# Optimization experiments

Measured on AMD Instinct MI355X. Metric: run time of the kernel, lower is better.

Reference implementation:

```python
import jax, jax.numpy as jnp
import numpy as np

B, N, C, H = 2, 2048, 1024, 16
D = C // H  # head_dim = 64


def setup_inputs() -> dict:
    key = jax.random.key(0)
    ks = jax.random.split(key, 5)
    s = 1.0 / np.sqrt(C)
    return {
        "q": jax.random.normal(ks[0], (B, N, C), dtype=jnp.float32),
        "W_qkv": jax.random.normal(ks[1], (C, 3 * C), dtype=jnp.float32) * s,
        "b_qkv": jnp.zeros((3 * C,), dtype=jnp.float32),
        "W_proj": jax.random.normal(ks[2], (C, C), dtype=jnp.float32) * s,
        "b_proj": jnp.zeros((C,), dtype=jnp.float32),
    }


def reference(q, W_qkv, b_qkv, W_proj, b_proj):
    # Self-attention: k = v = q. Full 3C projection (as in the torch code).
    qkv = q @ W_qkv + b_qkv  # [B, N, 3C]
    qh = qkv[:, :, :C].reshape(B, N, H, D)
    kh = qkv[:, :, C:2 * C].reshape(B, N, H, D)
    vh = qkv[:, :, 2 * C:].reshape(B, N, H, D)
    scale = D ** -0.5
    # [B, H, N, N] attention logits
    attn = jnp.einsum("bnhd,bmhd->bhnm", qh, kh) * scale
    attn = jax.nn.softmax(attn, axis=-1)
    out = jnp.einsum("bhnm,bmhd->bnhd", attn, vh).reshape(B, N, C)
    return out @ W_proj + b_proj
```

## Files before the change

### kernel.cpp

```cpp
#include <hip/hip_runtime.h>
#include <stdint.h>

typedef __bf16 bf16_t;
typedef __bf16 bf16x8 __attribute__((ext_vector_type(8)));
typedef __bf16 bf16x4 __attribute__((ext_vector_type(4)));
typedef float f32x4 __attribute__((ext_vector_type(4)));

#define L2E 1.44269504088896340736f
#define QSCALE (0.125f * L2E)

__device__ __forceinline__ void gload16(const bf16_t* g, bf16_t* l) {
  __builtin_amdgcn_global_load_lds(
      (const __attribute__((address_space(1))) void*)g,
      (__attribute__((address_space(3))) void*)l, 16, 0, 0);
}

__global__ __launch_bounds__(256) void cast_q_kernel(const float* __restrict__ in,
                                                     bf16_t* __restrict__ out) {
  int i = blockIdx.x * 256 + threadIdx.x;
  float4 v = reinterpret_cast<const float4*>(in)[i];
  bf16x4 o;
  o[0] = (bf16_t)v.x; o[1] = (bf16_t)v.y; o[2] = (bf16_t)v.z; o[3] = (bf16_t)v.w;
  reinterpret_cast<bf16x4*>(out)[i] = o;
}

__global__ __launch_bounds__(256) void transpose_cast_kernel(const float* __restrict__ in,
                                                             bf16_t* __restrict__ out,
                                                             int K, int N) {
  __shared__ float tile[64][65];
  int k0 = blockIdx.y * 64, n0 = blockIdx.x * 64;
  int t = threadIdx.x;
  int r = t >> 4, c4 = (t & 15) * 4;
#pragma unroll
  for (int rr = 0; rr < 4; rr++) {
    int row = r + rr * 16;
    float4 v = *reinterpret_cast<const float4*>(&in[(size_t)(k0 + row) * N + n0 + c4]);
    tile[row][c4 + 0] = v.x; tile[row][c4 + 1] = v.y;
    tile[row][c4 + 2] = v.z; tile[row][c4 + 3] = v.w;
  }
  __syncthreads();
#pragma unroll
  for (int rr = 0; rr < 4; rr++) {
    int nr = r + rr * 16;
    bf16x4 o;
#pragma unroll
    for (int i = 0; i < 4; i++) o[i] = (bf16_t)tile[c4 + i][nr];
    *reinterpret_cast<bf16x4*>(&out[(size_t)(n0 + nr) * K + k0 + c4]) = o;
  }
}

template <int MODE>
__global__ __launch_bounds__(256) void gemm_kernel(const bf16_t* __restrict__ A,
                                                   const bf16_t* __restrict__ Bt,
                                                   const float* __restrict__ bias,
                                                   void* __restrict__ out,
                                                   bf16_t* __restrict__ vT,
                                                   int K, int gm, int gn, int ldo) {
  __shared__ __align__(16) bf16_t smem[17408];
  bf16_t* At = smem;
  bf16_t* Bts = smem + 8192;
  const int t = threadIdx.x, lane = t & 63, w = t >> 6;
  const int g = lane >> 4, q = lane & 15;
  const int bid = blockIdx.x, x = bid & 7, r = bid >> 3;
  const int qm = gm >> 2, qn = gn >> 1;
  const int lm = r % qm, ln = r / qm;
  const int m0 = ((x & 3) * qm + lm) * 128, n0 = ((x >> 2) * qn + ln) * 128;
  const int wm = (w >> 1) * 64, wn = (w & 1) * 64;

  const bf16_t* srcA[4]; const bf16_t* srcB[4]; int dsto[4];
#pragma unroll
  for (int i = 0; i < 4; i++) {
    int gI = i * 256 + t;
    int row = gI >> 3, p = (gI & 7) ^ (row & 7);
    srcA[i] = A + (size_t)(m0 + row) * K + p * 8;
    srcB[i] = Bt + (size_t)(n0 + row) * K + p * 8;
    dsto[i] = (i * 256 + w * 64) * 8;
  }

  f32x4 acc[4][4];
#pragma unroll
  for (int i = 0; i < 4; i++)
#pragma unroll
    for (int j = 0; j < 4; j++) acc[i][j] = (f32x4){0.f, 0.f, 0.f, 0.f};

  for (int k0 = 0; k0 < K; k0 += 64) {
    __syncthreads();
#pragma unroll
    for (int i = 0; i < 4; i++) {
      gload16(srcA[i] + k0, &At[dsto[i]]);
      gload16(srcB[i] + k0, &Bts[dsto[i]]);
    }
    __syncthreads();
#pragma unroll
    for (int dc = 0; dc < 2; dc++) {
      bf16x8 am[4], bn[4];
#pragma unroll
      for (int i = 0; i < 4; i++) {
        int ra = wm + 16 * i + q;
        am[i] = *reinterpret_cast<const bf16x8*>(&At[ra * 64 + ((dc * 32 + g * 8) ^ ((ra & 7) * 8))]);
        int rb = wn + 16 * i + q;
        bn[i] = *reinterpret_cast<const bf16x8*>(&Bts[rb * 64 + ((dc * 32 + g * 8) ^ ((rb & 7) * 8))]);
      }
      __builtin_amdgcn_s_setprio(1);
#pragma unroll
      for (int i = 0; i < 4; i++)
#pragma unroll
        for (int j = 0; j < 4; j++)
          acc[i][j] = __builtin_amdgcn_mfma_f32_16x16x32_bf16(am[i], bn[j], acc[i][j], 0, 0, 0);
      __builtin_amdgcn_s_setprio(0);
    }
  }

  if (MODE == 0 && n0 >= 2048) {
    __syncthreads();
    bf16_t* TT = smem;
#pragma unroll
    for (int i = 0; i < 4; i++)
#pragma unroll
      for (int j = 0; j < 4; j++)
#pragma unroll
        for (int rr = 0; rr < 4; rr++) {
          int ch = wn + 16 * j + q;
          int tok = wm + 16 * i + 4 * g + rr;
          float v = acc[i][j][rr] + bias[n0 + ch];
          TT[ch * 136 + (((tok >> 3) ^ (ch & 7)) * 8) + (tok & 7)] = (bf16_t)v;
        }
    __syncthreads();
    const int bb = m0 >> 11;
    const int t0 = m0 & 2047;
#pragma unroll
    for (int it = 0; it < 8; it++) {
      int ch = it * 16 + w * 4 + (lane >> 4);
      int ck = lane & 15;
      uint4 val = *reinterpret_cast<const uint4*>(&TT[ch * 136 + ((ck ^ (ch & 7)) * 8)]);
      int vch = (n0 - 2048) + ch;
      bf16_t* dst = vT + ((size_t)(bb * 16 + (vch >> 6)) * 64 + (vch & 63)) * 2048 + t0 + ck * 8;
      *reinterpret_cast<uint4*>(dst) = val;
    }
  } else {
#pragma unroll
    for (int i = 0; i < 4; i++)
#pragma unroll
      for (int j = 0; j < 4; j++)
#pragma unroll
        for (int rr = 0; rr < 4; rr++) {
          int row = m0 + wm + 16 * i + 4 * g + rr;
          int col = n0 + wn + 16 * j + q;
          float v = acc[i][j][rr] + bias[col];
          if (MODE == 0) {
            if (col < 1024) v *= QSCALE;
            ((bf16_t*)out)[(size_t)row * ldo + col] = (bf16_t)v;
          } else {
            ((float*)out)[(size_t)row * ldo + col] = v;
          }
        }
  }
}

__global__ __launch_bounds__(256) void attn_kernel(const bf16_t* __restrict__ qk,
                                                   const bf16_t* __restrict__ vT,
                                                   bf16_t* __restrict__ aout) {
  __shared__ __align__(16) bf16_t sK[2][4096];
  __shared__ __align__(16) bf16_t sV[2][4096];
  __shared__ __align__(16) bf16_t sP[4][1024];

  const int t = threadIdx.x, lane = t & 63, w = t >> 6;
  const int g = lane >> 4, q = lane & 15;
  const int bid = blockIdx.x, xr = bid >> 3;
  const int bh = (bid & 7) * 4 + (xr >> 5);
  const int b = bh >> 4, h = bh & 15;
  const int q0 = (xr & 31) * 64 + w * 16;
  const bf16_t* qk_b = qk + (size_t)b * 2048 * 2048;
  const bf16_t* vT_h = vT + (size_t)bh * 64 * 2048;
  bf16_t* Pw = sP[w];

  const bf16_t* srcK[2]; const bf16_t* srcV[2]; int dsto[2];
#pragma unroll
  for (int i = 0; i < 2; i++) {
    int gI = (w * 2 + i) * 64 + lane;
    int row = gI >> 3, p = (gI & 7) ^ (row & 7);
    srcK[i] = qk_b + (size_t)row * 2048 + 1024 + h * 64 + p * 8;
    srcV[i] = vT_h + (size_t)row * 2048 + p * 8;
    dsto[i] = (w * 2 + i) * 512;
  }

  bf16x8 bq[2];
  {
    const bf16_t* qr = qk_b + (size_t)(q0 + q) * 2048 + h * 64;
    bq[0] = *reinterpret_cast<const bf16x8*>(qr + g * 8);
    bq[1] = *reinterpret_cast<const bf16x8*>(qr + 32 + g * 8);
  }

  bf16x8 ones;
#pragma unroll
  for (int i = 0; i < 8; i++) ones[i] = (bf16_t)1.0f;

  f32x4 oacc[4];
#pragma unroll
  for (int c = 0; c < 4; c++) oacc[c] = (f32x4){0.f, 0.f, 0.f, 0.f};
  f32x4 lacc = (f32x4){0.f, 0.f, 0.f, 0.f};

#pragma unroll
  for (int i = 0; i < 2; i++) {
    gload16(srcK[i], &sK[0][dsto[i]]);
    gload16(srcV[i], &sV[0][dsto[i]]);
  }
  __syncthreads();

  for (int tt = 0; tt < 32; tt++) {
    const int cur = tt & 1;
    if (tt + 1 < 32) {
      size_t koffK = (size_t)(tt + 1) * 64 * 2048;
      size_t koffV = (size_t)(tt + 1) * 64;
#pragma unroll
      for (int i = 0; i < 2; i++) {
        gload16(srcK[i] + koffK, &sK[cur ^ 1][dsto[i]]);
        gload16(srcV[i] + koffV, &sV[cur ^ 1][dsto[i]]);
      }
    }

    const bf16_t* Kc = sK[cur];
    f32x4 s[4];
    __builtin_amdgcn_s_setprio(1);
#pragma unroll
    for (int c = 0; c < 4; c++) {
      int row = 16 * c + q, sw = (q & 7) * 8;
      bf16x8 ka0 = *reinterpret_cast<const bf16x8*>(&Kc[row * 64 + ((g * 8) ^ sw)]);
      bf16x8 ka1 = *reinterpret_cast<const bf16x8*>(&Kc[row * 64 + ((32 + g * 8) ^ sw)]);
      f32x4 z = (f32x4){0.f, 0.f, 0.f, 0.f};
      z = __builtin_amdgcn_mfma_f32_16x16x32_bf16(ka0, bq[0], z, 0, 0, 0);
      z = __builtin_amdgcn_mfma_f32_16x16x32_bf16(ka1, bq[1], z, 0, 0, 0);
      s[c] = z;
    }
    __builtin_amdgcn_s_setprio(0);

#pragma unroll
    for (int c = 0; c < 4; c++) {
      bf16x4 pk;
#pragma unroll
      for (int rr = 0; rr < 4; rr++) pk[rr] = (bf16_t)exp2f(s[c][rr]);
      *reinterpret_cast<bf16x4*>(
          &Pw[q * 64 + (((2 * c + (g >> 1)) ^ (q & 7)) * 8) + (g & 1) * 4]) = pk;
    }

    const bf16_t* Vc = sV[cur];
    __builtin_amdgcn_s_setprio(1);
#pragma unroll
    for (int kc = 0; kc < 2; kc++) {
      bf16x8 pb = *reinterpret_cast<const bf16x8*>(
          &Pw[q * 64 + (((kc * 4 + g) ^ (q & 7)) * 8)]);
      lacc = __builtin_amdgcn_mfma_f32_16x16x32_bf16(ones, pb, lacc, 0, 0, 0);
#pragma unroll
      for (int c = 0; c < 4; c++) {
        int row = 16 * c + q;
        bf16x8 va = *reinterpret_cast<const bf16x8*>(
            &Vc[row * 64 + (((kc * 4 + g) ^ (q & 7)) * 8)]);
        oacc[c] = __builtin_amdgcn_mfma_f32_16x16x32_bf16(va, pb, oacc[c], 0, 0, 0);
      }
    }
    __builtin_amdgcn_s_setprio(0);

    __syncthreads();
  }

  float inv = 1.0f / lacc[0];
  bf16_t* orow = aout + (size_t)(b * 2048 + q0 + q) * 1024 + h * 64;
#pragma unroll
  for (int c = 0; c < 4; c++) {
    bf16x4 ov;
#pragma unroll
    for (int rr = 0; rr < 4; rr++) ov[rr] = (bf16_t)(oacc[c][rr] * inv);
    *reinterpret_cast<bf16x4*>(orow + c * 16 + g * 4) = ov;
  }
}

extern "C" void kernel_launch(void* const* d_in, const int* in_sizes, int n_in,
                              void* d_out, int out_size, void* d_ws, size_t ws_size,
                              hipStream_t stream) {
  const float* q     = (const float*)d_in[0];
  const float* Wqkv  = (const float*)d_in[1];
  const float* bqkv  = (const float*)d_in[2];
  const float* Wproj = (const float*)d_in[3];
  const float* bproj = (const float*)d_in[4];
  float* out = (float*)d_out;

  char* ws = (char*)d_ws;
  bf16_t* q_bf    = (bf16_t*)(ws);
  bf16_t* wqkv_t  = (bf16_t*)(ws + 8388608);
  bf16_t* wproj_t = (bf16_t*)(ws + 14680064);
  bf16_t* qk      = (bf16_t*)(ws + 16777216);
  bf16_t* vT      = (bf16_t*)(ws + 33554432);
  bf16_t* aout    = q_bf;

  cast_q_kernel<<<4096, 256, 0, stream>>>(q, q_bf);
  transpose_cast_kernel<<<dim3(48, 16), 256, 0, stream>>>(Wqkv, wqkv_t, 1024, 3072);
  transpose_cast_kernel<<<dim3(16, 16), 256, 0, stream>>>(Wproj, wproj_t, 1024, 1024);
  gemm_kernel<0><<<768, 256, 0, stream>>>(q_bf, wqkv_t, bqkv, qk, vT, 1024, 32, 24, 2048);
  attn_kernel<<<1024, 256, 0, stream>>>(qk, vT, aout);
  gemm_kernel<1><<<256, 256, 0, stream>>>(aout, wproj_t, bproj, out, nullptr, 1024, 32, 8, 1024);
}
```

Before: 149.4 us.

## Process two query sub-tiles per attention wave and use smaller projection GEMM tiles

Measured after the change: 145.6 us. -2.6%, faster.

```diff
diff --git a/kernel.cpp b/kernel.cpp
--- a/kernel.cpp
+++ b/kernel.cpp
@@ -49,61 +49,68 @@
   }
 }
 
-template <int MODE>
+template <int MODE, int BM>
 __global__ __launch_bounds__(256) void gemm_kernel(const bf16_t* __restrict__ A,
                                                    const bf16_t* __restrict__ Bt,
                                                    const float* __restrict__ bias,
                                                    void* __restrict__ out,
                                                    bf16_t* __restrict__ vT,
                                                    int K, int gm, int gn, int ldo) {
-  __shared__ __align__(16) bf16_t smem[17408];
+  constexpr int ACH = BM / 8;
+  constexpr int NCH = ACH + 16;
+  constexpr int CPW = NCH / 4;
+  constexpr int IR = BM / 32;
+  constexpr int SMEM = (MODE == 0) ? 17408 : (BM * 64 + 8192);
+  __shared__ __align__(16) bf16_t smem[SMEM];
   bf16_t* At = smem;
-  bf16_t* Bts = smem + 8192;
+  bf16_t* Bts = smem + BM * 64;
   const int t = threadIdx.x, lane = t & 63, w = t >> 6;
   const int g = lane >> 4, q = lane & 15;
   const int bid = blockIdx.x, x = bid & 7, r = bid >> 3;
   const int qm = gm >> 2, qn = gn >> 1;
   const int lm = r % qm, ln = r / qm;
-  const int m0 = ((x & 3) * qm + lm) * 128, n0 = ((x >> 2) * qn + ln) * 128;
-  const int wm = (w >> 1) * 64, wn = (w & 1) * 64;
-
-  const bf16_t* srcA[4]; const bf16_t* srcB[4]; int dsto[4];
-#pragma unroll
-  for (int i = 0; i < 4; i++) {
-    int gI = i * 256 + t;
-    int row = gI >> 3, p = (gI & 7) ^ (row & 7);
-    srcA[i] = A + (size_t)(m0 + row) * K + p * 8;
-    srcB[i] = Bt + (size_t)(n0 + row) * K + p * 8;
-    dsto[i] = (i * 256 + w * 64) * 8;
-  }
-
-  f32x4 acc[4][4];
-#pragma unroll
-  for (int i = 0; i < 4; i++)
+  const int m0 = ((x & 3) * qm + lm) * BM, n0 = ((x >> 2) * qn + ln) * 128;
+  const int wm = (w >> 1) * (BM / 2), wn = (w & 1) * 64;
+
+  const bf16_t* srcp[CPW]; int dsto[CPW];
+#pragma unroll
+  for (int i = 0; i < CPW; i++) {
+    int cI = i * 4 + w;
+    bool isA = cI < ACH;
+    int row = (isA ? cI : cI - ACH) * 8 + (lane >> 3);
+    int p = (lane & 7) ^ (row & 7);
+    srcp[i] = (isA ? A + (size_t)(m0 + row) * K : Bt + (size_t)(n0 + row) * K) + p * 8;
+    dsto[i] = (isA ? cI * 512 : BM * 64 + (cI - ACH) * 512) - (size_t)lane * 8;
+    dsto[i] = (isA ? cI * 512 : BM * 64 + (cI - ACH) * 512);
+  }
+
+  f32x4 acc[IR][4];
+#pragma unroll
+  for (int i = 0; i < IR; i++)
 #pragma unroll
     for (int j = 0; j < 4; j++) acc[i][j] = (f32x4){0.f, 0.f, 0.f, 0.f};
 
   for (int k0 = 0; k0 < K; k0 += 64) {
     __syncthreads();
 #pragma unroll
-    for (int i = 0; i < 4; i++) {
-      gload16(srcA[i] + k0, &At[dsto[i]]);
-      gload16(srcB[i] + k0, &Bts[dsto[i]]);
-    }
+    for (int i = 0; i < CPW; i++) gload16(srcp[i] + k0, &smem[dsto[i]]);
     __syncthreads();
 #pragma unroll
     for (int dc = 0; dc < 2; dc++) {
-      bf16x8 am[4], bn[4];
-#pragma unroll
-      for (int i = 0; i < 4; i++) {
+      bf16x8 am[IR], bn[4];
+#pragma unroll
+      for (int i = 0; i < IR; i++) {
         int ra = wm + 16 * i + q;
         am[i] = *reinterpret_cast<const bf16x8*>(&At[ra * 64 + ((dc * 32 + g * 8) ^ ((ra & 7) * 8))]);
-        int rb = wn + 16 * i + q;
-        bn[i] = *reinterpret_cast<const bf16x8*>(&Bts[rb * 64 + ((dc * 32 + g * 8) ^ ((rb & 7) * 8))]);
+      }
+#pragma unroll
+      for (int j = 0; j < 4; j++) {
+        int rb = wn + 16 * j + q;
+        bn[j] = *reinterpret_cast<const bf16x8*>(&Bts[rb * 64 + ((dc * 32 + g * 8) ^ ((rb & 7) * 8))]);
       }
       __builtin_amdgcn_s_setprio(1);
 #pragma unroll
-      for (int i = 0; i < 4; i++)
+      for (int i = 0; i < IR; i++)
 #pragma unroll
         for (int j = 0; j < 4; j++)
           acc[i][j] = __builtin_amdgcn_mfma_f32_16x16x32_bf16(am[i], bn[j], acc[i][j], 0, 0, 0);
@@ -115,7 +122,7 @@
     __syncthreads();
     bf16_t* TT = smem;
 #pragma unroll
-    for (int i = 0; i < 4; i++)
+    for (int i = 0; i < IR; i++)
 #pragma unroll
       for (int j = 0; j < 4; j++)
 #pragma unroll
@@ -139,7 +146,7 @@
     }
   } else {
 #pragma unroll
-    for (int i = 0; i < 4; i++)
+    for (int i = 0; i < IR; i++)
 #pragma unroll
       for (int j = 0; j < 4; j++)
 #pragma unroll
@@ -162,14 +169,14 @@
                                                    bf16_t* __restrict__ aout) {
   __shared__ __align__(16) bf16_t sK[2][4096];
   __shared__ __align__(16) bf16_t sV[2][4096];
-  __shared__ __align__(16) bf16_t sP[4][1024];
+  __shared__ __align__(16) bf16_t sP[4][2048];
 
   const int t = threadIdx.x, lane = t & 63, w = t >> 6;
   const int g = lane >> 4, q = lane & 15;
   const int bid = blockIdx.x, xr = bid >> 3;
-  const int bh = (bid & 7) * 4 + (xr >> 5);
+  const int bh = (bid & 7) * 4 + (xr >> 4);
   const int b = bh >> 4, h = bh & 15;
-  const int q0 = (xr & 31) * 64 + w * 16;
+  const int q0 = (xr & 15) * 128 + w * 16;
   const bf16_t* qk_b = qk + (size_t)b * 2048 * 2048;
   const bf16_t* vT_h = vT + (size_t)bh * 64 * 2048;
   bf16_t* Pw = sP[w];
@@ -184,21 +191,26 @@
     dsto[i] = (w * 2 + i) * 512;
   }
 
-  bf16x8 bq[2];
-  {
-    const bf16_t* qr = qk_b + (size_t)(q0 + q) * 2048 + h * 64;
-    bq[0] = *reinterpret_cast<const bf16x8*>(qr + g * 8);
-    bq[1] = *reinterpret_cast<const bf16x8*>(qr + 32 + g * 8);
+  bf16x8 bq[2][2];
+#pragma unroll
+  for (int s = 0; s < 2; s++) {
+    const bf16_t* qr = qk_b + (size_t)(q0 + s * 64 + q) * 2048 + h * 64;
+    bq[s][0] = *reinterpret_cast<const bf16x8*>(qr + g * 8);
+    bq[s][1] = *reinterpret_cast<const bf16x8*>(qr + 32 + g * 8);
   }
 
   bf16x8 ones;
 #pragma unroll
   for (int i = 0; i < 8; i++) ones[i] = (bf16_t)1.0f;
 
-  f32x4 oacc[4];
-#pragma unroll
-  for (int c = 0; c < 4; c++) oacc[c] = (f32x4){0.f, 0.f, 0.f, 0.f};
-  f32x4 lacc = (f32x4){0.f, 0.f, 0.f, 0.f};
+  f32x4 oacc[2][4];
+#pragma unroll
+  for (int s = 0; s < 2; s++)
+#pragma unroll
+    for (int c = 0; c < 4; c++) oacc[s][c] = (f32x4){0.f, 0.f, 0.f, 0.f};
+  f32x4 lacc[2];
+  lacc[0] = (f32x4){0.f, 0.f, 0.f, 0.f};
+  lacc[1] = (f32x4){0.f, 0.f, 0.f, 0.f};
 
 #pragma unroll
   for (int i = 0; i < 2; i++) {
@@ -220,42 +232,55 @@
     }
 
     const bf16_t* Kc = sK[cur];
-    f32x4 s[4];
-    __builtin_amdgcn_s_setprio(1);
+    bf16x8 kf[4][2];
 #pragma unroll
     for (int c = 0; c < 4; c++) {
       int row = 16 * c + q, sw = (q & 7) * 8;
-      bf16x8 ka0 = *reinterpret_cast<const bf16x8*>(&Kc[row * 64 + ((g * 8) ^ sw)]);
-      bf16x8 ka1 = *reinterpret_cast<const bf16x8*>(&Kc[row * 64 + ((32 + g * 8) ^ sw)]);
+      kf[c][0] = *reinterpret_cast<const bf16x8*>(&Kc[row * 64 + ((g * 8) ^ sw)]);
+      kf[c][1] = *reinterpret_cast<const bf16x8*>(&Kc[row * 64 + ((32 + g * 8) ^ sw)]);
+    }
+    f32x4 s0[4], s1[4];
+    __builtin_amdgcn_s_setprio(1);
+#pragma unroll
+    for (int c = 0; c < 4; c++) {
       f32x4 z = (f32x4){0.f, 0.f, 0.f, 0.f};
-      z = __builtin_amdgcn_mfma_f32_16x16x32_bf16(ka0, bq[0], z, 0, 0, 0);
-      z = __builtin_amdgcn_mfma_f32_16x16x32_bf16(ka1, bq[1], z, 0, 0, 0);
-      s[c] = z;
+      z = __builtin_amdgcn_mfma_f32_16x16x32_bf16(kf[c][0], bq[0][0], z, 0, 0, 0);
+      s0[c] = __builtin_amdgcn_mfma_f32_16x16x32_bf16(kf[c][1], bq[0][1], z, 0, 0, 0);
+      f32x4 z1 = (f32x4){0.f, 0.f, 0.f, 0.f};
+      z1 = __builtin_amdgcn_mfma_f32_16x16x32_bf16(kf[c][0], bq[1][0], z1, 0, 0, 0);
+      s1[c] = __builtin_amdgcn_mfma_f32_16x16x32_bf16(kf[c][1], bq[1][1], z1, 0, 0, 0);
     }
     __builtin_amdgcn_s_setprio(0);
 
 #pragma unroll
     for (int c = 0; c < 4; c++) {
-      bf16x4 pk;
-#pragma unroll
-      for (int rr = 0; rr < 4; rr++) pk[rr] = (bf16_t)exp2f(s[c][rr]);
-      *reinterpret_cast<bf16x4*>(
-          &Pw[q * 64 + (((2 * c + (g >> 1)) ^ (q & 7)) * 8) + (g & 1) * 4]) = pk;
+      bf16x4 pk0, pk1;
+#pragma unroll
+      for (int rr = 0; rr < 4; rr++) {
+        pk0[rr] = (bf16_t)exp2f(s0[c][rr]);
+        pk1[rr] = (bf16_t)exp2f(s1[c][rr]);
+      }
+      int off = q * 64 + (((2 * c + (g >> 1)) ^ (q & 7)) * 8) + (g & 1) * 4;
+      *reinterpret_cast<bf16x4*>(&Pw[off]) = pk0;
+      *reinterpret_cast<bf16x4*>(&Pw[1024 + off]) = pk1;
     }
 
     const bf16_t* Vc = sV[cur];
     __builtin_amdgcn_s_setprio(1);
 #pragma unroll
     for (int kc = 0; kc < 2; kc++) {
-      bf16x8 pb = *reinterpret_cast<const bf16x8*>(
-          &Pw[q * 64 + (((kc * 4 + g) ^ (q & 7)) * 8)]);
-      lacc = __builtin_amdgcn_mfma_f32_16x16x32_bf16(ones, pb, lacc, 0, 0, 0);
+      int poff = q * 64 + (((kc * 4 + g) ^ (q & 7)) * 8);
+      bf16x8 pb0 = *reinterpret_cast<const bf16x8*>(&Pw[poff]);
+      bf16x8 pb1 = *reinterpret_cast<const bf16x8*>(&Pw[1024 + poff]);
+      lacc[0] = __builtin_amdgcn_mfma_f32_16x16x32_bf16(ones, pb0, lacc[0], 0, 0, 0);
+      lacc[1] = __builtin_amdgcn_mfma_f32_16x16x32_bf16(ones, pb1, lacc[1], 0, 0, 0);
 #pragma unroll
       for (int c = 0; c < 4; c++) {
         int row = 16 * c + q;
         bf16x8 va = *reinterpret_cast<const bf16x8*>(
             &Vc[row * 64 + (((kc * 4 + g) ^ (q & 7)) * 8)]);
-        oacc[c] = __builtin_amdgcn_mfma_f32_16x16x32_bf16(va, pb, oacc[c], 0, 0, 0);
+        oacc[0][c] = __builtin_amdgcn_mfma_f32_16x16x32_bf16(va, pb0, oacc[0][c], 0, 0, 0);
+        oacc[1][c] = __builtin_amdgcn_mfma_f32_16x16x32_bf16(va, pb1, oacc[1][c], 0, 0, 0);
       }
     }
     __builtin_amdgcn_s_setprio(0);
@@ -263,14 +288,17 @@
     __syncthreads();
   }
 
-  float inv = 1.0f / lacc[0];
-  bf16_t* orow = aout + (size_t)(b * 2048 + q0 + q) * 1024 + h * 64;
-#pragma unroll
-  for (int c = 0; c < 4; c++) {
-    bf16x4 ov;
-#pragma unroll
-    for (int rr = 0; rr < 4; rr++) ov[rr] = (bf16_t)(oacc[c][rr] * inv);
-    *reinterpret_cast<bf16x4*>(orow + c * 16 + g * 4) = ov;
+#pragma unroll
+  for (int s = 0; s < 2; s++) {
+    float inv = 1.0f / lacc[s][0];
+    bf16_t* orow = aout + (size_t)(b * 2048 + q0 + s * 64 + q) * 1024 + h * 64;
+#pragma unroll
+    for (int c = 0; c < 4; c++) {
+      bf16x4 ov;
+#pragma unroll
+      for (int rr = 0; rr < 4; rr++) ov[rr] = (bf16_t)(oacc[s][c][rr] * inv);
+      *reinterpret_cast<bf16x4*>(orow + c * 16 + g * 4) = ov;
+    }
   }
 }
 
@@ -295,7 +323,7 @@
   cast_q_kernel<<<4096, 256, 0, stream>>>(q, q_bf);
   transpose_cast_kernel<<<dim3(48, 16), 256, 0, stream>>>(Wqkv, wqkv_t, 1024, 3072);
   transpose_cast_kernel<<<dim3(16, 16), 256, 0, stream>>>(Wproj, wproj_t, 1024, 1024);
-  gemm_kernel<0><<<768, 256, 0, stream>>>(q_bf, wqkv_t, bqkv, qk, vT, 1024, 32, 24, 2048);
-  attn_kernel<<<1024, 256, 0, stream>>>(qk, vT, aout);
-  gemm_kernel<1><<<256, 256, 0, stream>>>(aout, wproj_t, bproj, out, nullptr, 1024, 32, 8, 1024);
-}
+  gemm_kernel<0, 128><<<768, 256, 0, stream>>>(q_bf, wqkv_t, bqkv, qk, vT, 1024, 32, 24, 2048);
+  attn_kernel<<<512, 256, 0, stream>>>(qk, vT, aout);
+  gemm_kernel<1, 64><<<512, 256, 0, stream>>>(aout, wproj_t, bproj, out, nullptr, 1024, 64, 8, 1024);
+}
```
